# Performance work log

Measured on AMD Instinct MI355X. Metric: run time of the kernel, lower is better.

Reference implementation:

```python
import jax, jax.numpy as jnp
import numpy as np

NF, DG, K = 32, 8, 9  # channels, deformable groups, kernel taps (3x3)


def conv2d(x, w, b, stride=1):
    out = jax.lax.conv_general_dilated(x, w, (stride, stride), ((1, 1), (1, 1)),
                                       dimension_numbers=('NCHW', 'OIHW', 'NCHW'))
    return out + b[None, :, None, None]


def lrelu(x):
    return jnp.where(x >= 0, x, 0.1 * x)


def dcn(x, off_fea, om_w, om_b, w, b):
    """Modulated deformable conv v2 (DCN_sep): offsets/mask predicted from off_fea."""
    B, C, H, W = x.shape
    om = conv2d(off_fea, om_w, om_b).reshape(B, DG, 3, K, H, W)
    off_y, off_x = om[:, :, 0], om[:, :, 1]          # [B,DG,K,H,W]
    mask = jax.nn.sigmoid(om[:, :, 2])               # [B,DG,K,H,W]
    ky = (jnp.arange(K) // 3 - 1).astype(x.dtype)    # kernel tap dy in {-1,0,1}
    kx = (jnp.arange(K) % 3 - 1).astype(x.dtype)
    py = off_y + jnp.arange(H, dtype=x.dtype)[:, None] + ky[:, None, None]
    px = off_x + jnp.arange(W, dtype=x.dtype) + kx[:, None, None]
    y0 = jnp.floor(py); x0 = jnp.floor(px)
    dy = py - y0; dx = px - x0
    Cg = C // DG
    xg = x.reshape(B, DG, Cg, H * W)

    def gather(yi, xi):
        valid = ((yi >= 0) & (yi <= H - 1) & (xi >= 0) & (xi <= W - 1)).astype(x.dtype)
        idx = (jnp.clip(yi, 0, H - 1).astype(jnp.int32) * W
               + jnp.clip(xi, 0, W - 1).astype(jnp.int32)).reshape(B, DG, 1, K * H * W)
        v = jnp.take_along_axis(xg, idx, axis=3).reshape(B, DG, Cg, K, H, W)
        return v * valid[:, :, None]  # zero padding outside

    samp = (gather(y0, x0) * ((1 - dy) * (1 - dx))[:, :, None]
            + gather(y0, x0 + 1) * ((1 - dy) * dx)[:, :, None]
            + gather(y0 + 1, x0) * (dy * (1 - dx))[:, :, None]
            + gather(y0 + 1, x0 + 1) * (dy * dx)[:, :, None])
    samp = samp * mask[:, :, None]                   # modulation
    out = jnp.einsum('bgckhw,ogck->bohw', samp, w.reshape(w.shape[0], DG, Cg, K))
    return out + b[None, :, None, None]


def _forward(L1_fea, L1_offset, L2_offset, L3_offset, offset,
             w_l2c1, b_l2c1, w_l2c2, b_l2c2, w_l3c1, b_l3c1, w_l3c2, b_l3c2,
             w_l2fea, b_l2fea, w_l1fea, b_l1fea,
             l3_om_w, l3_om_b, l3_w, l3_b,
             l2_om_w, l2_om_b, l2_w, l2_b,
             l1_om_w, l1_om_b, l1_w, l1_b,
             cas_om_w, cas_om_b, cas_w, cas_b):
    B, C, H, W = L1_fea.shape
    # pyramid feature extraction
    L2 = lrelu(conv2d(L1_fea, w_l2c1, b_l2c1, 2))
    L2 = lrelu(conv2d(L2, w_l2c2, b_l2c2))
    L3 = lrelu(conv2d(L2, w_l3c1, b_l3c1, 2))
    L3 = lrelu(conv2d(L3, w_l3c2, b_l3c2))
    # PCD alignment: coarse-to-fine
    L3f = lrelu(dcn(L3, L3_offset, l3_om_w, l3_om_b, l3_w, l3_b))
    L2f = dcn(L2, L2_offset, l2_om_w, l2_om_b, l2_w, l2_b)
    L3u = jax.image.resize(L3f, (B, C, H // 2, W // 2), 'bilinear')
    L2f = lrelu(conv2d(jnp.concatenate([L2f, L3u], 1), w_l2fea, b_l2fea))
    L1f = dcn(L1_fea, L1_offset, l1_om_w, l1_om_b, l1_w, l1_b)
    L2u = jax.image.resize(L2f, (B, C, H, W), 'bilinear')
    L1f = conv2d(jnp.concatenate([L1f, L2u], 1), w_l1fea, b_l1fea)
    return lrelu(dcn(L1f, offset, cas_om_w, cas_om_b, cas_w, cas_b))


def setup_inputs() -> dict:
    key = jax.random.key(0)
    ks = iter(jax.random.split(key, 64))
    def nrm(shape, s=1.0):
        return jax.random.normal(next(ks), shape, jnp.float32) * s
    B, H, W = 4, 192, 192
    inp = {
        'L1_fea': nrm((B, NF, H, W)),
        'L1_offset': nrm((B, NF, H, W)),
        'L2_offset': nrm((B, NF, H // 2, W // 2)),
        'L3_offset': nrm((B, NF, H // 4, W // 4)),
        'offset': nrm((B, NF, H, W)),
    }
    cs = 1.0 / float(np.sqrt(NF * 9))
    for n, sh in [('w_l2c1', (NF, NF, 3, 3)), ('w_l2c2', (NF, NF, 3, 3)),
                  ('w_l3c1', (NF, NF, 3, 3)), ('w_l3c2', (NF, NF, 3, 3)),
                  ('w_l2fea', (NF, 2 * NF, 3, 3)), ('w_l1fea', (NF, 2 * NF, 3, 3))]:
        inp[n] = nrm(sh, cs)
        inp[n.replace('w_', 'b_')] = jnp.zeros((NF,), jnp.float32)
    for p in ['l3', 'l2', 'l1', 'cas']:
        inp[p + '_om_w'] = nrm((DG * 3 * K, NF, 3, 3), 0.01)  # small => offsets of a few px
        inp[p + '_om_b'] = jnp.zeros((DG * 3 * K,), jnp.float32)
        inp[p + '_w'] = nrm((NF, NF, 3, 3), cs)
        inp[p + '_b'] = jnp.zeros((NF,), jnp.float32)
    return inp


def reference(L1_fea, L1_offset, L2_offset, L3_offset, offset,
              w_l2c1, b_l2c1, w_l2c2, b_l2c2, w_l3c1, b_l3c1, w_l3c2, b_l3c2,
              w_l2fea, b_l2fea, w_l1fea, b_l1fea,
              l3_om_w, l3_om_b, l3_w, l3_b,
              l2_om_w, l2_om_b, l2_w, l2_b,
              l1_om_w, l1_om_b, l1_w, l1_b,
              cas_om_w, cas_om_b, cas_w, cas_b):
    return _forward(L1_fea, L1_offset, L2_offset, L3_offset, offset,
                    w_l2c1, b_l2c1, w_l2c2, b_l2c2, w_l3c1, b_l3c1, w_l3c2, b_l3c2,
                    w_l2fea, b_l2fea, w_l1fea, b_l1fea,
                    l3_om_w, l3_om_b, l3_w, l3_b,
                    l2_om_w, l2_om_b, l2_w, l2_b,
                    l1_om_w, l1_om_b, l1_w, l1_b,
                    cas_om_w, cas_om_b, cas_w, cas_b)
```

## Files before the change

### kernel.cpp

```cpp
#include <hip/hip_runtime.h>
#include <math.h>

#define NFC 32
#define DGC 8

#define CDIV(a, b) (((a) + (b) - 1) / (b))

typedef __attribute__((ext_vector_type(8))) short bf16x8;
typedef __attribute__((ext_vector_type(4))) float f32x4;

__device__ __forceinline__ unsigned short f2bf(float f) {
    unsigned int u = __float_as_uint(f);
    u += 0x7fffu + ((u >> 16) & 1u);
    return (unsigned short)(u >> 16);
}
__device__ __forceinline__ float bf2f(unsigned short s) {
    return __uint_as_float((unsigned int)s << 16);
}
__device__ __forceinline__ float bf_lo(unsigned int u) { return __uint_as_float(u << 16); }
__device__ __forceinline__ float bf_hi(unsigned int u) { return __uint_as_float(u & 0xffff0000u); }

struct Ptr4F { const float* s[4]; };
struct Ptr4U { unsigned short* d[4]; };

__global__ void k_swz_om4(Ptr4F src, Ptr4U dst) {
    const float* w = src.s[blockIdx.y];
    unsigned short* o = dst.d[blockIdx.y];
    int i = blockIdx.x * 256 + threadIdx.x;
    if (i >= 9 * 14 * 64 * 8) return;
    int j  = i & 7;
    int l  = (i >> 3) & 63;
    int nt = (i >> 9) % 14;
    int t  = i / (14 * 512);
    int n  = nt * 16 + (l & 15);
    int ic = (l >> 4) * 8 + j;
    float v = (n < 216) ? w[((size_t)(n * 32 + ic)) * 9 + t] : 0.f;
    o[i] = f2bf(v);
}

template<int ICt>
__global__ void k_swz_wA(Ptr4F src, Ptr4U dst) {
    const int KC = ICt / 32;
    const float* w = src.s[blockIdx.y];
    unsigned short* o = dst.d[blockIdx.y];
    int i = blockIdx.x * 256 + threadIdx.x;
    if (i >= 9 * KC * 1024) return;
    int idx = i;
    int j = idx & 7;   idx >>= 3;
    int l = idx & 63;  idx >>= 6;
    int mt = idx & 1;  idx >>= 1;
    int ck = idx % KC; idx /= KC;
    int t = idx;
    int oc = mt * 16 + (l & 15);
    int ic = ck * 32 + (l >> 4) * 8 + j;
    o[i] = f2bf(w[((size_t)(oc * ICt + ic)) * 9 + t]);
}

__global__ void k_swz_wmA4(Ptr4F src, Ptr4U dst) {
    const float* w = src.s[blockIdx.y];
    unsigned short* o = dst.d[blockIdx.y];
    int i = blockIdx.x * 256 + threadIdx.x;
    if (i >= 9216) return;
    int j  = i & 7;
    int l  = (i >> 3) & 63;
    int mt = (i >> 9) & 1;
    int kc = i >> 10;
    int oc = mt * 16 + (l & 15);
    int k  = kc * 32 + (l >> 4) * 8 + j;
    int ic = k / 9, t = k % 9;
    o[i] = f2bf(w[((size_t)(oc * 32 + ic)) * 9 + t]);
}

__global__ void k_cvt_nhwc(Ptr4F src, Ptr4U dst, int HW, int Btot) {
    const float* in = src.s[blockIdx.y];
    unsigned short* out = dst.d[blockIdx.y];
    int i = blockIdx.x * 256 + threadIdx.x;
    if (i >= Btot * HW * 32) return;
    int c = i & 31;
    int pxf = i >> 5;
    int b = pxf / HW;
    int hw = pxf % HW;
    out[i] = f2bf(in[((size_t)(b * 32 + c)) * HW + hw]);
}

template<int NT, int KC, int STRIDE, bool LRELU>
__global__ __launch_bounds__(256)
void k_conv_mfma(const unsigned short* __restrict__ in1,
                 const unsigned short* __restrict__ in2,
                 const unsigned short* __restrict__ wA,
                 const float* __restrict__ bias,
                 unsigned short* __restrict__ out,
                 int B, int Hin, int Win, int Hout, int Wout) {
    int wid  = (blockIdx.x * 256 + threadIdx.x) >> 6;
    int lane = threadIdx.x & 63;
    int strips = Wout / (16 * NT);
    if (wid >= B * Hout * strips) return;
    int st = wid % strips;
    int h  = (wid / strips) % Hout;
    int b  = wid / (strips * Hout);
    int px0 = st * 16 * NT;

    f32x4 acc[NT][2];
#pragma unroll
    for (int nt = 0; nt < NT; ++nt)
#pragma unroll
        for (int mt = 0; mt < 2; ++mt)
#pragma unroll
            for (int r = 0; r < 4; ++r) acc[nt][mt][r] = 0.f;

    int n  = lane & 15;
    int kq = lane >> 4;

#pragma unroll
    for (int t = 0; t < 9; ++t) {
        int hy = h * STRIDE + t / 3 - 1;
        if (hy < 0 || hy >= Hin) continue;
#pragma unroll
        for (int ck = 0; ck < KC; ++ck) {
            const unsigned short* rowp =
                ((KC == 2 && ck == 1) ? in2 : in1) + ((size_t)(b * Hin + hy) * Win) * 32;
            bf16x8 a0 = *(const bf16x8*)(wA + (size_t)((((t * KC + ck) * 2 + 0) * 64 + lane)) * 8);
            bf16x8 a1 = *(const bf16x8*)(wA + (size_t)((((t * KC + ck) * 2 + 1) * 64 + lane)) * 8);
#pragma unroll
            for (int nt = 0; nt < NT; ++nt) {
                int wx = (px0 + nt * 16 + n) * STRIDE + t % 3 - 1;
                bf16x8 bf;
#pragma unroll
                for (int j = 0; j < 8; ++j) bf[j] = 0;
                if (wx >= 0 && wx < Win)
                    bf = *(const bf16x8*)(rowp + (size_t)wx * 32 + kq * 8);
                acc[nt][0] = __builtin_amdgcn_mfma_f32_16x16x32_bf16(a0, bf, acc[nt][0], 0, 0, 0);
                acc[nt][1] = __builtin_amdgcn_mfma_f32_16x16x32_bf16(a1, bf, acc[nt][1], 0, 0, 0);
            }
        }
    }

    size_t rowbase = ((size_t)(b * Hout + h) * Wout);
#pragma unroll
    for (int mt = 0; mt < 2; ++mt) {
        float4 bs = *(const float4*)(bias + mt * 16 + kq * 4);
#pragma unroll
        for (int nt = 0; nt < NT; ++nt) {
            int px = px0 + nt * 16 + n;
            float v0 = acc[nt][mt][0] + bs.x;
            float v1 = acc[nt][mt][1] + bs.y;
            float v2 = acc[nt][mt][2] + bs.z;
            float v3 = acc[nt][mt][3] + bs.w;
            if (LRELU) {
                v0 = (v0 >= 0.f) ? v0 : 0.1f * v0;
                v1 = (v1 >= 0.f) ? v1 : 0.1f * v1;
                v2 = (v2 >= 0.f) ? v2 : 0.1f * v2;
                v3 = (v3 >= 0.f) ? v3 : 0.1f * v3;
            }
            ushort4 sv = make_ushort4(f2bf(v0), f2bf(v1), f2bf(v2), f2bf(v3));
            *(ushort4*)(out + (rowbase + px) * 32 + mt * 16 + kq * 4) = sv;
        }
    }
}

__global__ __launch_bounds__(256)
void k_gemm_om(const unsigned short* __restrict__ offn,
               const unsigned short* __restrict__ wswz,
               unsigned short* __restrict__ om,
               int B, int H, int W) {
    int wid  = (blockIdx.x * 256 + threadIdx.x) >> 6;
    int lane = threadIdx.x & 63;
    int mtW = W >> 4;
    if (wid >= B * H * mtW) return;
    int mt = wid % mtW;
    int h  = (wid / mtW) % H;
    int b  = wid / (mtW * H);
    int Npx = B * H * W;
    int px0 = mt * 16;

    f32x4 acc[14];
#pragma unroll
    for (int nt = 0; nt < 14; ++nt)
#pragma unroll
        for (int r = 0; r < 4; ++r) acc[nt][r] = 0.f;

    int m  = lane & 15;
    int kq = lane >> 4;

    for (int t = 0; t < 9; ++t) {
        int hy = h + t / 3 - 1;
        if (hy < 0 || hy >= H) continue;
        int wx = px0 + m + t % 3 - 1;
        bf16x8 a;
#pragma unroll
        for (int j = 0; j < 8; ++j) a[j] = 0;
        if (wx >= 0 && wx < W)
            a = *(const bf16x8*)(offn + (((size_t)(b * H + hy) * W + wx) << 5) + kq * 8);
        const unsigned short* wp = wswz + ((size_t)t * 14 * 64 + lane) * 8;
#pragma unroll
        for (int nt = 0; nt < 14; ++nt) {
            bf16x8 bfrag = *(const bf16x8*)(wp + (size_t)nt * 64 * 8);
            acc[nt] = __builtin_amdgcn_mfma_f32_16x16x32_bf16(a, bfrag, acc[nt], 0, 0, 0);
        }
    }

    int ch_lo = lane & 15;
    int pxb = (b * H + h) * W + px0 + (lane >> 4) * 4;
#pragma unroll
    for (int nt = 0; nt < 14; ++nt) {
        int ch = nt * 16 + ch_lo;
        if (ch < 216) {
            ushort4 v = make_ushort4(f2bf(acc[nt][0]), f2bf(acc[nt][1]),
                                     f2bf(acc[nt][2]), f2bf(acc[nt][3]));
            *(ushort4*)(om + (size_t)ch * Npx + pxb) = v;
        }
    }
}

template<int MODE>
__global__ __launch_bounds__(256)
void k_sample_conv(const unsigned short* __restrict__ xn,
                   const unsigned short* __restrict__ om,
                   const float* __restrict__ om_b,
                   const unsigned short* __restrict__ wmA,
                   const float* __restrict__ bias,
                   float* __restrict__ outf,
                   unsigned short* __restrict__ outb,
                   int B, int H, int W) {
    const int ROW = 296;
    __shared__ __align__(16) unsigned short s_samp[32 * ROW];

    int tid = threadIdx.x;
    int px = tid & 31, g = tid >> 5;
    int Npx = B * H * W;
    int px0 = blockIdx.x * 32;

    {
        int idx = px0 + px;
        int w = idx % W;
        int h = (idx / W) % H;
        int b = idx / (W * H);

        float om27[27];
#pragma unroll
        for (int j = 0; j < 27; ++j)
            om27[j] = bf2f(om[(size_t)(g * 27 + j) * Npx + idx]) + om_b[g * 27 + j];

        const unsigned short* xb = xn + ((size_t)b * H * W) * 32 + g * 4;
        float Hm1 = (float)(H - 1), Wm1 = (float)(W - 1);
        unsigned short arr[36];

#pragma unroll
        for (int k = 0; k < 9; ++k) {
            float mval = 1.f / (1.f + __expf(-om27[18 + k]));
            float py  = om27[k]     + (float)(h + k / 3 - 1);
            float pxx = om27[9 + k] + (float)(w + k % 3 - 1);
            float y0f = floorf(py), x0f = floorf(pxx);
            float dy = py - y0f, dx = pxx - x0f;
            float y1f = y0f + 1.f, x1f = x0f + 1.f;
            float vy0 = (y0f >= 0.f && y0f <= Hm1) ? 1.f : 0.f;
            float vy1 = (y1f >= 0.f && y1f <= Hm1) ? 1.f : 0.f;
            float vx0 = (x0f >= 0.f && x0f <= Wm1) ? 1.f : 0.f;
            float vx1 = (x1f >= 0.f && x1f <= Wm1) ? 1.f : 0.f;
            float w00 = (1.f - dy) * (1.f - dx) * vy0 * vx0;
            float w01 = (1.f - dy) * dx * vy0 * vx1;
            float w10 = dy * (1.f - dx) * vy1 * vx0;
            float w11 = dy * dx * vy1 * vx1;
            int y0c = (int)fminf(fmaxf(y0f, 0.f), Hm1);
            int y1c = (int)fminf(fmaxf(y1f, 0.f), Hm1);
            int x0c = (int)fminf(fmaxf(x0f, 0.f), Wm1);
            int x1c = (int)fminf(fmaxf(x1f, 0.f), Wm1);

            uint2 u00 = *(const uint2*)(xb + ((size_t)y0c * W + x0c) * 32);
            uint2 u01 = *(const uint2*)(xb + ((size_t)y0c * W + x1c) * 32);
            uint2 u10 = *(const uint2*)(xb + ((size_t)y1c * W + x0c) * 32);
            uint2 u11 = *(const uint2*)(xb + ((size_t)y1c * W + x1c) * 32);

            arr[0 * 9 + k] = f2bf((w00 * bf_lo(u00.x) + w01 * bf_lo(u01.x) +
                                   w10 * bf_lo(u10.x) + w11 * bf_lo(u11.x)) * mval);
            arr[1 * 9 + k] = f2bf((w00 * bf_hi(u00.x) + w01 * bf_hi(u01.x) +
                                   w10 * bf_hi(u10.x) + w11 * bf_hi(u11.x)) * mval);
            arr[2 * 9 + k] = f2bf((w00 * bf_lo(u00.y) + w01 * bf_lo(u01.y) +
                                   w10 * bf_lo(u10.y) + w11 * bf_lo(u11.y)) * mval);
            arr[3 * 9 + k] = f2bf((w00 * bf_hi(u00.y) + w01 * bf_hi(u01.y) +
                                   w10 * bf_hi(u10.y) + w11 * bf_hi(u11.y)) * mval);
        }
        ushort4* dst = (ushort4*)(s_samp + px * ROW + g * 36);
        const ushort4* srcp = (const ushort4*)arr;
#pragma unroll
        for (int q = 0; q < 9; ++q) dst[q] = srcp[q];
    }
    __syncthreads();

    int lane = tid & 63;
    int wsid = tid >> 6;
    int mt = wsid & 1, nt = wsid >> 1;

    f32x4 acc;
#pragma unroll
    for (int r = 0; r < 4; ++r) acc[r] = 0.f;

    const unsigned short* sb = s_samp + (nt * 16 + (lane & 15)) * ROW + (lane >> 4) * 8;
#pragma unroll
    for (int kc = 0; kc < 9; ++kc) {
        bf16x8 a   = *(const bf16x8*)(wmA + ((size_t)(kc * 2 + mt) * 64 + lane) * 8);
        bf16x8 bfr = *(const bf16x8*)(sb + kc * 32);
        acc = __builtin_amdgcn_mfma_f32_16x16x32_bf16(a, bfr, acc, 0, 0, 0);
    }

    int pxg = px0 + nt * 16 + (lane & 15);
    int kq = lane >> 4;
    float4 bs = *(const float4*)(bias + mt * 16 + kq * 4);
    float v[4] = {acc[0] + bs.x, acc[1] + bs.y, acc[2] + bs.z, acc[3] + bs.w};
    if (MODE >= 1) {
#pragma unroll
        for (int r = 0; r < 4; ++r) v[r] = (v[r] >= 0.f) ? v[r] : 0.1f * v[r];
    }
    if (MODE == 2) {
        int w2 = pxg % W, h2 = (pxg / W) % H, b2 = pxg / (W * H);
#pragma unroll
        for (int r = 0; r < 4; ++r) {
            int oc = mt * 16 + kq * 4 + r;
            outf[((size_t)(b2 * 32 + oc) * H + h2) * W + w2] = v[r];
        }
    } else {
        ushort4 sv = make_ushort4(f2bf(v[0]), f2bf(v[1]), f2bf(v[2]), f2bf(v[3]));
        *(ushort4*)(outb + (size_t)pxg * 32 + mt * 16 + kq * 4) = sv;
    }
}

__global__ void k_resize2x_nhwc(const unsigned short* __restrict__ in,
                                unsigned short* __restrict__ out,
                                int B, int Hin, int Win) {
    int Hout = Hin * 2, Wout = Win * 2;
    int i = blockIdx.x * 256 + threadIdx.x;
    int total = B * Hout * Wout * 4;
    if (i >= total) return;
    int q  = i & 3;
    int wo = (i >> 2) % Wout;
    int ho = (i >> 2) / Wout % Hout;
    int b  = (i >> 2) / (Wout * Hout);
    float fy = 0.5f * (float)ho - 0.25f;
    float fx = 0.5f * (float)wo - 0.25f;
    float y0f = floorf(fy), x0f = floorf(fx);
    float wy1 = fy - y0f, wx1 = fx - x0f;
    int y0 = max(0, min((int)y0f, Hin - 1));
    int y1 = max(0, min((int)y0f + 1, Hin - 1));
    int x0 = max(0, min((int)x0f, Win - 1));
    int x1 = max(0, min((int)x0f + 1, Win - 1));
    const unsigned short* base = in + ((size_t)b * Hin * Win) * 32 + q * 8;
    const uint4 u00 = *(const uint4*)(base + ((size_t)y0 * Win + x0) * 32);
    const uint4 u01 = *(const uint4*)(base + ((size_t)y0 * Win + x1) * 32);
    const uint4 u10 = *(const uint4*)(base + ((size_t)y1 * Win + x0) * 32);
    const uint4 u11 = *(const uint4*)(base + ((size_t)y1 * Win + x1) * 32);
    float c00 = (1.f - wy1) * (1.f - wx1), c01 = (1.f - wy1) * wx1;
    float c10 = wy1 * (1.f - wx1), c11 = wy1 * wx1;
    const unsigned int* p00 = (const unsigned int*)&u00;
    const unsigned int* p01 = (const unsigned int*)&u01;
    const unsigned int* p10 = (const unsigned int*)&u10;
    const unsigned int* p11 = (const unsigned int*)&u11;
    unsigned int packed[4];
#pragma unroll
    for (int d = 0; d < 4; ++d) {
        float lo = c00 * bf_lo(p00[d]) + c01 * bf_lo(p01[d]) +
                   c10 * bf_lo(p10[d]) + c11 * bf_lo(p11[d]);
        float hi = c00 * bf_hi(p00[d]) + c01 * bf_hi(p01[d]) +
                   c10 * bf_hi(p10[d]) + c11 * bf_hi(p11[d]);
        packed[d] = (unsigned int)f2bf(lo) | ((unsigned int)f2bf(hi) << 16);
    }
    *(uint4*)(out + ((size_t)(b * Hout + ho) * Wout + wo) * 32 + q * 8) =
        make_uint4(packed[0], packed[1], packed[2], packed[3]);
}

extern "C" void kernel_launch(void* const* d_in, const int* in_sizes, int n_in,
                              void* d_out, int out_size, void* d_ws, size_t ws_size,
                              hipStream_t stream) {
    const float* L1_fea = (const float*)d_in[0];
    const float* L1_off = (const float*)d_in[1];
    const float* L2_off = (const float*)d_in[2];
    const float* L3_off = (const float*)d_in[3];
    const float* offset = (const float*)d_in[4];
    const float* w_l2c1 = (const float*)d_in[5];   const float* b_l2c1 = (const float*)d_in[6];
    const float* w_l2c2 = (const float*)d_in[7];   const float* b_l2c2 = (const float*)d_in[8];
    const float* w_l3c1 = (const float*)d_in[9];   const float* b_l3c1 = (const float*)d_in[10];
    const float* w_l3c2 = (const float*)d_in[11];  const float* b_l3c2 = (const float*)d_in[12];
    const float* w_l2fea = (const float*)d_in[13]; const float* b_l2fea = (const float*)d_in[14];
    const float* w_l1fea = (const float*)d_in[15]; const float* b_l1fea = (const float*)d_in[16];
    const float* l3_om_w = (const float*)d_in[17]; const float* l3_om_b = (const float*)d_in[18];
    const float* l3_w = (const float*)d_in[19];    const float* l3_b = (const float*)d_in[20];
    const float* l2_om_w = (const float*)d_in[21]; const float* l2_om_b = (const float*)d_in[22];
    const float* l2_w = (const float*)d_in[23];    const float* l2_b = (const float*)d_in[24];
    const float* l1_om_w = (const float*)d_in[25]; const float* l1_om_b = (const float*)d_in[26];
    const float* l1_w = (const float*)d_in[27];    const float* l1_b = (const float*)d_in[28];
    const float* cas_om_w = (const float*)d_in[29]; const float* cas_om_b = (const float*)d_in[30];
    const float* cas_w = (const float*)d_in[31];   const float* cas_b = (const float*)d_in[32];

    const int B = 4, H1 = 192, W1 = 192, H2 = 96, W2 = 96, H3 = 48, W3 = 48;
    const int HW1 = H1 * W1, HW2 = H2 * W2, HW3 = H3 * W3;

    char* ws = (char*)d_ws;
    size_t cur = 0;
    auto alloc = [&](size_t bytes) {
        char* p = ws + cur;
        cur += (bytes + 255) & ~(size_t)255;
        return p;
    };

    unsigned short* wA_l2c1  = (unsigned short*)alloc(9216 * 2);
    unsigned short* wA_l2c2  = (unsigned short*)alloc(9216 * 2);
    unsigned short* wA_l3c1  = (unsigned short*)alloc(9216 * 2);
    unsigned short* wA_l3c2  = (unsigned short*)alloc(9216 * 2);
    unsigned short* wA_l2fea = (unsigned short*)alloc(18432 * 2);
    unsigned short* wA_l1fea = (unsigned short*)alloc(18432 * 2);
    unsigned short* wmA_l3   = (unsigned short*)alloc(9216 * 2);
    unsigned short* wmA_l2   = (unsigned short*)alloc(9216 * 2);
    unsigned short* wmA_l1   = (unsigned short*)alloc(9216 * 2);
    unsigned short* wmA_cas  = (unsigned short*)alloc(9216 * 2);
    unsigned short* wswz_l3  = (unsigned short*)alloc(64512 * 2);
    unsigned short* wswz_l2  = (unsigned short*)alloc(64512 * 2);
    unsigned short* wswz_l1  = (unsigned short*)alloc(64512 * 2);
    unsigned short* wswz_cas = (unsigned short*)alloc(64512 * 2);

    unsigned short* offn_l3  = (unsigned short*)alloc((size_t)B * 32 * HW3 * 2);
    unsigned short* offn_l2  = (unsigned short*)alloc((size_t)B * 32 * HW2 * 2);
    unsigned short* offn_l1  = (unsigned short*)alloc((size_t)B * 32 * HW1 * 2);
    unsigned short* offn_cas = (unsigned short*)alloc((size_t)B * 32 * HW1 * 2);
    unsigned short* xn_l1    = (unsigned short*)alloc((size_t)B * 32 * HW1 * 2);
    unsigned short* L2a      = (unsigned short*)alloc((size_t)B * 32 * HW2 * 2);
    unsigned short* L2n      = (unsigned short*)alloc((size_t)B * 32 * HW2 * 2);
    unsigned short* L3a      = (unsigned short*)alloc((size_t)B * 32 * HW3 * 2);
    unsigned short* L3n      = (unsigned short*)alloc((size_t)B * 32 * HW3 * 2);
    unsigned short* L3f      = (unsigned short*)alloc((size_t)B * 32 * HW3 * 2);
    unsigned short* L2f_pre  = (unsigned short*)alloc((size_t)B * 32 * HW2 * 2);
    unsigned short* L3u      = (unsigned short*)alloc((size_t)B * 32 * HW2 * 2);
    unsigned short* L2f      = (unsigned short*)alloc((size_t)B * 32 * HW2 * 2);
    unsigned short* L1f_pre  = (unsigned short*)alloc((size_t)B * 32 * HW1 * 2);
    unsigned short* L2u      = (unsigned short*)alloc((size_t)B * 32 * HW1 * 2);
    unsigned short* L1f      = (unsigned short*)alloc((size_t)B * 32 * HW1 * 2);
    unsigned short* om       = (unsigned short*)alloc((size_t)224 * B * HW1 * 2);

    {
        Ptr4F s = {{l3_om_w, l2_om_w, l1_om_w, cas_om_w}};
        Ptr4U d = {{wswz_l3, wswz_l2, wswz_l1, wswz_cas}};
        k_swz_om4<<<dim3(CDIV(64512, 256), 4), 256, 0, stream>>>(s, d);
    }
    {
        Ptr4F s = {{w_l2c1, w_l2c2, w_l3c1, w_l3c2}};
        Ptr4U d = {{wA_l2c1, wA_l2c2, wA_l3c1, wA_l3c2}};
        k_swz_wA<32><<<dim3(CDIV(9216, 256), 4), 256, 0, stream>>>(s, d);
    }
    {
        Ptr4F s = {{w_l2fea, w_l1fea, nullptr, nullptr}};
        Ptr4U d = {{wA_l2fea, wA_l1fea, nullptr, nullptr}};
        k_swz_wA<64><<<dim3(CDIV(18432, 256), 2), 256, 0, stream>>>(s, d);
    }
    {
        Ptr4F s = {{l3_w, l2_w, l1_w, cas_w}};
        Ptr4U d = {{wmA_l3, wmA_l2, wmA_l1, wmA_cas}};
        k_swz_wmA4<<<dim3(CDIV(9216, 256), 4), 256, 0, stream>>>(s, d);
    }

    {
        Ptr4F s = {{L1_off, offset, L1_fea, nullptr}};
        Ptr4U d = {{offn_l1, offn_cas, xn_l1, nullptr}};
        k_cvt_nhwc<<<dim3(CDIV(B * 32 * HW1, 256), 3), 256, 0, stream>>>(s, d, HW1, B);
    }
    {
        Ptr4F s = {{L2_off, nullptr, nullptr, nullptr}};
        Ptr4U d = {{offn_l2, nullptr, nullptr, nullptr}};
        k_cvt_nhwc<<<dim3(CDIV(B * 32 * HW2, 256), 1), 256, 0, stream>>>(s, d, HW2, B);
    }
    {
        Ptr4F s = {{L3_off, nullptr, nullptr, nullptr}};
        Ptr4U d = {{offn_l3, nullptr, nullptr, nullptr}};
        k_cvt_nhwc<<<dim3(CDIV(B * 32 * HW3, 256), 1), 256, 0, stream>>>(s, d, HW3, B);
    }

    k_conv_mfma<3, 1, 2, true><<<CDIV(B * H2 * 2, 4), 256, 0, stream>>>(
        xn_l1, nullptr, wA_l2c1, b_l2c1, L2a, B, H1, W1, H2, W2);
    k_conv_mfma<3, 1, 1, true><<<CDIV(B * H2 * 2, 4), 256, 0, stream>>>(
        L2a, nullptr, wA_l2c2, b_l2c2, L2n, B, H2, W2, H2, W2);
    k_conv_mfma<3, 1, 2, true><<<CDIV(B * H3 * 1, 4), 256, 0, stream>>>(
        L2n, nullptr, wA_l3c1, b_l3c1, L3a, B, H2, W2, H3, W3);
    k_conv_mfma<3, 1, 1, true><<<CDIV(B * H3 * 1, 4), 256, 0, stream>>>(
        L3a, nullptr, wA_l3c2, b_l3c2, L3n, B, H3, W3, H3, W3);

    k_gemm_om<<<CDIV(B * H3 * (W3 / 16), 4), 256, 0, stream>>>(offn_l3, wswz_l3, om, B, H3, W3);
    k_sample_conv<1><<<B * HW3 / 32, 256, 0, stream>>>(
        L3n, om, l3_om_b, wmA_l3, l3_b, nullptr, L3f, B, H3, W3);

    k_gemm_om<<<CDIV(B * H2 * (W2 / 16), 4), 256, 0, stream>>>(offn_l2, wswz_l2, om, B, H2, W2);
    k_sample_conv<0><<<B * HW2 / 32, 256, 0, stream>>>(
        L2n, om, l2_om_b, wmA_l2, l2_b, nullptr, L2f_pre, B, H2, W2);
    k_resize2x_nhwc<<<CDIV(B * HW2 * 4, 256), 256, 0, stream>>>(L3f, L3u, B, H3, W3);
    k_conv_mfma<3, 2, 1, true><<<CDIV(B * H2 * 2, 4), 256, 0, stream>>>(
        L2f_pre, L3u, wA_l2fea, b_l2fea, L2f, B, H2, W2, H2, W2);

    k_gemm_om<<<CDIV(B * H1 * (W1 / 16), 4), 256, 0, stream>>>(offn_l1, wswz_l1, om, B, H1, W1);
    k_sample_conv<0><<<B * HW1 / 32, 256, 0, stream>>>(
        xn_l1, om, l1_om_b, wmA_l1, l1_b, nullptr, L1f_pre, B, H1, W1);
    k_resize2x_nhwc<<<CDIV(B * HW1 * 4, 256), 256, 0, stream>>>(L2f, L2u, B, H2, W2);
    k_conv_mfma<4, 2, 1, false><<<CDIV(B * H1 * 3, 4), 256, 0, stream>>>(
        L1f_pre, L2u, wA_l1fea, b_l1fea, L1f, B, H1, W1, H1, W1);

    k_gemm_om<<<CDIV(B * H1 * (W1 / 16), 4), 256, 0, stream>>>(offn_cas, wswz_cas, om, B, H1, W1);
    k_sample_conv<2><<<B * HW1 / 32, 256, 0, stream>>>(
        L1f, om, cas_om_b, wmA_cas, cas_b, (float*)d_out, nullptr, B, H1, W1);
}
```

Measured before the change: 611.9 us.

## Fuse offset/mask conv GEMM into deformable sampling kernel via shared memory

Each DCN stage previously ran two kernels: one computed the 216-channel offset/mask map into a global buffer, and a second read it back to do bilinear sampling and the output conv. Now a single kernel computes the offset map for its 32-pixel tile with MFMA, keeping it in LDS. The tile's four waves split the 14 output-channel tiles between them. This removes the global write and read of the offset map and four kernel launches. The cost is extra LDS use per block, which may lower occupancy, and each wave now has less MFMA work per weight fragment load.

```diff
diff --git a/kernel.cpp b/kernel.cpp
--- a/kernel.cpp
+++ b/kernel.cpp
@@ -158,79 +158,92 @@
     }
 }
 
-__global__ __launch_bounds__(256)
-void k_gemm_om(const unsigned short* __restrict__ offn,
-               const unsigned short* __restrict__ wswz,
-               unsigned short* __restrict__ om,
-               int B, int H, int W) {
-    int wid  = (blockIdx.x * 256 + threadIdx.x) >> 6;
-    int lane = threadIdx.x & 63;
-    int mtW = W >> 4;
-    if (wid >= B * H * mtW) return;
-    int mt = wid % mtW;
-    int h  = (wid / mtW) % H;
-    int b  = wid / (mtW * H);
-    int Npx = B * H * W;
-    int px0 = mt * 16;
-
-    f32x4 acc[14];
-#pragma unroll
-    for (int nt = 0; nt < 14; ++nt)
-#pragma unroll
-        for (int r = 0; r < 4; ++r) acc[nt][r] = 0.f;
-
-    int m  = lane & 15;
-    int kq = lane >> 4;
-
-    for (int t = 0; t < 9; ++t) {
-        int hy = h + t / 3 - 1;
-        if (hy < 0 || hy >= H) continue;
-        int wx = px0 + m + t % 3 - 1;
-        bf16x8 a;
-#pragma unroll
-        for (int j = 0; j < 8; ++j) a[j] = 0;
-        if (wx >= 0 && wx < W)
-            a = *(const bf16x8*)(offn + (((size_t)(b * H + hy) * W + wx) << 5) + kq * 8);
-        const unsigned short* wp = wswz + ((size_t)t * 14 * 64 + lane) * 8;
-#pragma unroll
-        for (int nt = 0; nt < 14; ++nt) {
-            bf16x8 bfrag = *(const bf16x8*)(wp + (size_t)nt * 64 * 8);
-            acc[nt] = __builtin_amdgcn_mfma_f32_16x16x32_bf16(a, bfrag, acc[nt], 0, 0, 0);
-        }
-    }
-
-    int ch_lo = lane & 15;
-    int pxb = (b * H + h) * W + px0 + (lane >> 4) * 4;
-#pragma unroll
-    for (int nt = 0; nt < 14; ++nt) {
-        int ch = nt * 16 + ch_lo;
-        if (ch < 216) {
-            ushort4 v = make_ushort4(f2bf(acc[nt][0]), f2bf(acc[nt][1]),
-                                     f2bf(acc[nt][2]), f2bf(acc[nt][3]));
-            *(ushort4*)(om + (size_t)ch * Npx + pxb) = v;
-        }
-    }
-}
-
 template<int MODE>
 __global__ __launch_bounds__(256)
-void k_sample_conv(const unsigned short* __restrict__ xn,
-                   const unsigned short* __restrict__ om,
-                   const float* __restrict__ om_b,
-                   const unsigned short* __restrict__ wmA,
-                   const float* __restrict__ bias,
-                   float* __restrict__ outf,
-                   unsigned short* __restrict__ outb,
-                   int B, int H, int W) {
+void k_dcn_fused(const unsigned short* __restrict__ offn,
+                 const unsigned short* __restrict__ wswz,
+                 const float* __restrict__ om_b,
+                 const unsigned short* __restrict__ xn,
+                 const unsigned short* __restrict__ wmA,
+                 const float* __restrict__ bias,
+                 float* __restrict__ outf,
+                 unsigned short* __restrict__ outb,
+                 int B, int H, int W) {
     const int ROW = 296;
+    const int OMR = 36;
+    __shared__ __align__(16) unsigned short s_om[216 * OMR];
     __shared__ __align__(16) unsigned short s_samp[32 * ROW];
 
     int tid = threadIdx.x;
-    int px = tid & 31, g = tid >> 5;
-    int Npx = B * H * W;
+    int lane = tid & 63;
+    int wv = tid >> 6;
     int px0 = blockIdx.x * 32;
 
     {
+        int n  = lane & 15;
+        int kq = lane >> 4;
+
+        int bmt[2], hmt[2], wmt[2];
+#pragma unroll
+        for (int mt = 0; mt < 2; ++mt) {
+            int p0 = px0 + mt * 16;
+            bmt[mt] = p0 / (H * W);
+            hmt[mt] = (p0 / W) % H;
+            wmt[mt] = p0 % W;
+        }
+
+        f32x4 acc[4][2];
+#pragma unroll
+        for (int i = 0; i < 4; ++i)
+#pragma unroll
+            for (int mt = 0; mt < 2; ++mt)
+#pragma unroll
+                for (int r = 0; r < 4; ++r) acc[i][mt][r] = 0.f;
+
+#pragma unroll
+        for (int t = 0; t < 9; ++t) {
+            bf16x8 a[2];
+#pragma unroll
+            for (int mt = 0; mt < 2; ++mt) {
+#pragma unroll
+                for (int j = 0; j < 8; ++j) a[mt][j] = 0;
+                int hy = hmt[mt] + t / 3 - 1;
+                int wx = wmt[mt] + n + t % 3 - 1;
+                if (hy >= 0 && hy < H && wx >= 0 && wx < W)
+                    a[mt] = *(const bf16x8*)(offn +
+                        (((size_t)(bmt[mt] * H + hy) * W + wx) << 5) + kq * 8);
+            }
+#pragma unroll
+            for (int i = 0; i < 4; ++i) {
+                int nt = wv * 4 + i;
+                if (nt < 14) {
+                    bf16x8 bf = *(const bf16x8*)(wswz + (((size_t)t * 14 + nt) * 64 + lane) * 8);
+                    acc[i][0] = __builtin_amdgcn_mfma_f32_16x16x32_bf16(a[0], bf, acc[i][0], 0, 0, 0);
+                    acc[i][1] = __builtin_amdgcn_mfma_f32_16x16x32_bf16(a[1], bf, acc[i][1], 0, 0, 0);
+                }
+            }
+        }
+
+#pragma unroll
+        for (int i = 0; i < 4; ++i) {
+            int nt = wv * 4 + i;
+            if (nt < 14) {
+                int ch = nt * 16 + n;
+                if (ch < 216) {
+#pragma unroll
+                    for (int mt = 0; mt < 2; ++mt) {
+                        ushort4 v = make_ushort4(f2bf(acc[i][mt][0]), f2bf(acc[i][mt][1]),
+                                                 f2bf(acc[i][mt][2]), f2bf(acc[i][mt][3]));
+                        *(ushort4*)(s_om + ch * OMR + mt * 16 + kq * 4) = v;
+                    }
+                }
+            }
+        }
+    }
+    __syncthreads();
+
+    {
+        int px = tid & 31, g = tid >> 5;
         int idx = px0 + px;
         int w = idx % W;
         int h = (idx / W) % H;
@@ -239,7 +252,7 @@
         float om27[27];
 #pragma unroll
         for (int j = 0; j < 27; ++j)
-            om27[j] = bf2f(om[(size_t)(g * 27 + j) * Npx + idx]) + om_b[g * 27 + j];
+            om27[j] = bf2f(s_om[(g * 27 + j) * OMR + px]) + om_b[g * 27 + j];
 
         const unsigned short* xb = xn + ((size_t)b * H * W) * 32 + g * 4;
         float Hm1 = (float)(H - 1), Wm1 = (float)(W - 1);
@@ -287,15 +300,14 @@
     }
     __syncthreads();
 
-    int lane = tid & 63;
     int wsid = tid >> 6;
-    int mt = wsid & 1, nt = wsid >> 1;
+    int mt = wsid & 1, nt2 = wsid >> 1;
 
     f32x4 acc;
 #pragma unroll
     for (int r = 0; r < 4; ++r) acc[r] = 0.f;
 
-    const unsigned short* sb = s_samp + (nt * 16 + (lane & 15)) * ROW + (lane >> 4) * 8;
+    const unsigned short* sb = s_samp + (nt2 * 16 + (lane & 15)) * ROW + (lane >> 4) * 8;
 #pragma unroll
     for (int kc = 0; kc < 9; ++kc) {
         bf16x8 a   = *(const bf16x8*)(wmA + ((size_t)(kc * 2 + mt) * 64 + lane) * 8);
@@ -303,7 +315,7 @@
         acc = __builtin_amdgcn_mfma_f32_16x16x32_bf16(a, bfr, acc, 0, 0, 0);
     }
 
-    int pxg = px0 + nt * 16 + (lane & 15);
+    int pxg = px0 + nt2 * 16 + (lane & 15);
     int kq = lane >> 4;
     float4 bs = *(const float4*)(bias + mt * 16 + kq * 4);
     float v[4] = {acc[0] + bs.x, acc[1] + bs.y, acc[2] + bs.z, acc[3] + bs.w};
@@ -432,7 +444,6 @@
     unsigned short* L1f_pre  = (unsigned short*)alloc((size_t)B * 32 * HW1 * 2);
     unsigned short* L2u      = (unsigned short*)alloc((size_t)B * 32 * HW1 * 2);
     unsigned short* L1f      = (unsigned short*)alloc((size_t)B * 32 * HW1 * 2);
-    unsigned short* om       = (unsigned short*)alloc((size_t)224 * B * HW1 * 2);
 
     {
         Ptr4F s = {{l3_om_w, l2_om_w, l1_om_w, cas_om_w}};
@@ -480,25 +491,21 @@
     k_conv_mfma<3, 1, 1, true><<<CDIV(B * H3 * 1, 4), 256, 0, stream>>>(
         L3a, nullptr, wA_l3c2, b_l3c2, L3n, B, H3, W3, H3, W3);
 
-    k_gemm_om<<<CDIV(B * H3 * (W3 / 16), 4), 256, 0, stream>>>(offn_l3, wswz_l3, om, B, H3, W3);
-    k_sample_conv<1><<<B * HW3 / 32, 256, 0, stream>>>(
-        L3n, om, l3_om_b, wmA_l3, l3_b, nullptr, L3f, B, H3, W3);
-
-    k_gemm_om<<<CDIV(B * H2 * (W2 / 16), 4), 256, 0, stream>>>(offn_l2, wswz_l2, om, B, H2, W2);
-    k_sample_conv<0><<<B * HW2 / 32, 256, 0, stream>>>(
-        L2n, om, l2_om_b, wmA_l2, l2_b, nullptr, L2f_pre, B, H2, W2);
+    k_dcn_fused<1><<<B * HW3 / 32, 256, 0, stream>>>(
+        offn_l3, wswz_l3, l3_om_b, L3n, wmA_l3, l3_b, nullptr, L3f, B, H3, W3);
+
+    k_dcn_fused<0><<<B * HW2 / 32, 256, 0, stream>>>(
+        offn_l2, wswz_l2, l2_om_b, L2n, wmA_l2, l2_b, nullptr, L2f_pre, B, H2, W2);
     k_resize2x_nhwc<<<CDIV(B * HW2 * 4, 256), 256, 0, stream>>>(L3f, L3u, B, H3, W3);
     k_conv_mfma<3, 2, 1, true><<<CDIV(B * H2 * 2, 4), 256, 0, stream>>>(
         L2f_pre, L3u, wA_l2fea, b_l2fea, L2f, B, H2, W2, H2, W2);
 
-    k_gemm_om<<<CDIV(B * H1 * (W1 / 16), 4), 256, 0, stream>>>(offn_l1, wswz_l1, om, B, H1, W1);
-    k_sample_conv<0><<<B * HW1 / 32, 256, 0, stream>>>(
-        xn_l1, om, l1_om_b, wmA_l1, l1_b, nullptr, L1f_pre, B, H1, W1);
+    k_dcn_fused<0><<<B * HW1 / 32, 256, 0, stream>>>(
+        offn_l1, wswz_l1, l1_om_b, xn_l1, wmA_l1, l1_b, nullptr, L1f_pre, B, H1, W1);
     k_resize2x_nhwc<<<CDIV(B * HW1 * 4, 256), 256, 0, stream>>>(L2f, L2u, B, H2, W2);
     k_conv_mfma<4, 2, 1, false><<<CDIV(B * H1 * 3, 4), 256, 0, stream>>>(
         L1f_pre, L2u, wA_l1fea, b_l1fea, L1f, B, H1, W1, H1, W1);
 
-    k_gemm_om<<<CDIV(B * H1 * (W1 / 16), 4), 256, 0, stream>>>(offn_cas, wswz_cas, om, B, H1, W1);
-    k_sample_conv<2><<<B * HW1 / 32, 256, 0, stream>>>(
-        L1f, om, cas_om_b, wmA_cas, cas_b, (float*)d_out, nullptr, B, H1, W1);
-}
+    k_dcn_fused<2><<<B * HW1 / 32, 256, 0, stream>>>(
+        offn_cas, wswz_cas, cas_om_b, L1f, wmA_cas, cas_b, (float*)d_out, nullptr, B, H1, W1);
+}
```

Result: no change. 606.8 us (-0.8%).
